# Optimization experiments

Hardware: AMD Instinct MI355X
Metric: run time of the kernel (lower is better)

Reference implementation:

```python
import jax, jax.numpy as jnp
import numpy as np

B, D, H = 256, 512, 256
K = 5
MARGIN = 1.0
TAU = 1.0
LAM_C = 0.01
LAM_E = 0.1
BETA = 0.1
LN_EPS = 1e-5


def _layernorm(x, g, b):
    mu = jnp.mean(x, axis=-1, keepdims=True)
    var = jnp.var(x, axis=-1, keepdims=True)
    return (x - mu) * jax.lax.rsqrt(var + LN_EPS) * g + b


def setup_inputs() -> dict:
    key = jax.random.key(0)
    ks = jax.random.split(key, 16)
    s = 0.02
    inp = {
        "outputs": jax.random.normal(ks[0], (B, 3, 64, 64), jnp.float32),
        "images": jax.random.normal(ks[1], (B, 3, 64, 64), jnp.float32),
        "f_orig": jax.random.normal(ks[2], (B, D), jnp.float32),
        "f_recon": jax.random.normal(ks[3], (B, D), jnp.float32),
        "cf1": jax.random.normal(ks[4], (B, 256, 8, 8), jnp.float32),
        "cf2": jax.random.normal(ks[5], (B, 512, 4, 4), jnp.float32),
        # EnergyNet encoder params
        "W1": jax.random.normal(ks[6], (D, H), jnp.float32) * s,
        "b1": jnp.zeros((H,), jnp.float32),
        "g1": jnp.ones((H,), jnp.float32),
        "be1": jnp.zeros((H,), jnp.float32),
        "W2": jax.random.normal(ks[7], (H, H), jnp.float32) * s,
        "b2": jnp.zeros((H,), jnp.float32),
        # EnergyNet interaction params
        "W3": jax.random.normal(ks[8], (3 * H, H), jnp.float32) * s,
        "b3": jnp.zeros((H,), jnp.float32),
        "g3": jnp.ones((H,), jnp.float32),
        "be3": jnp.zeros((H,), jnp.float32),
        "W4": jax.random.normal(ks[9], (H, H // 2), jnp.float32) * s,
        "b4": jnp.zeros((H // 2,), jnp.float32),
        "W5": jax.random.normal(ks[10], (H // 2, 1), jnp.float32) * s,
        "b5": jnp.zeros((1,), jnp.float32),
    }
    return inp


def _encoder(x, W1, b1, g1, be1, W2, b2):
    h = _layernorm(x @ W1 + b1, g1, be1)
    return jax.nn.relu(h) @ W2 + b2


def _energy_matrix(f1, f2, W1, b1, g1, be1, W2, b2, W3, b3, g3, be3, W4, b4, W5, b5):
    e1 = _encoder(f1, W1, b1, g1, be1, W2, b2)  # [B,H]
    e2 = _encoder(f2, W1, b1, g1, be1, W2, b2)  # [B,H]
    e1b = jnp.broadcast_to(e1[:, None, :], (B, B, H))
    e2b = jnp.broadcast_to(e2[None, :, :], (B, B, H))
    combined = jnp.concatenate([e1b, e2b, e1b * e2b], axis=-1)  # [B,B,3H]
    h = jax.nn.relu(_layernorm(combined @ W3 + b3, g3, be3))
    h = jax.nn.relu(h @ W4 + b4)
    return (h @ W5 + b5)[..., 0]  # [B,B]


def _topk_neighbors(f, k):
    fn = f / (jnp.linalg.norm(f, axis=1, keepdims=True))
    sim = fn @ fn.T
    sim = jnp.where(jnp.eye(f.shape[0], dtype=bool), -jnp.inf, sim)
    _, idx = jax.lax.top_k(sim, k)  # [B,k]
    onehot = jnp.zeros((f.shape[0], f.shape[0]), jnp.float32)
    rows = jnp.arange(f.shape[0])[:, None]
    return onehot.at[rows, idx].set(1.0)


def _entropy(x):
    xn = (x - x.min()) / (x.max() - x.min() + 1e-8)
    # torch.histc(bins=256, min=0, max=1): values at max go to last bin
    idx = jnp.clip(jnp.floor(xn.reshape(-1) * 256.0).astype(jnp.int32), 0, 255)
    hist = jnp.bincount(idx, length=256).astype(jnp.float32)
    p = hist / hist.sum()
    return -jnp.sum(p * jnp.log2(p + 1e-8))


def reference(outputs, images, f_orig, f_recon, cf1, cf2,
              W1, b1, g1, be1, W2, b2, W3, b3, g3, be3, W4, b4, W5, b5):
    # reconstruction loss
    recon = jnp.mean((outputs - images) ** 2)

    # energy margin loss
    E = _energy_matrix(f_orig, f_recon, W1, b1, g1, be1, W2, b2,
                       W3, b3, g3, be3, W4, b4, W5, b5)
    pos = jnp.diag(E)[:, None]
    losses = jax.nn.relu(MARGIN + E - pos)
    neg_mask = ~jnp.eye(B, dtype=bool)
    standard_loss = jnp.sum(losses * neg_mask) / (B * (B - 1))

    k = min(K, B - 1)
    on = _topk_neighbors(f_orig, k)
    rn = _topk_neighbors(f_recon, k)
    inter = jnp.sum(on * rn, axis=1)
    union = jnp.sum(jnp.clip(on + rn, 0.0, 1.0), axis=1)
    jaccard = inter / (union + 1e-8)
    neighbor_loss = 1.0 - jnp.mean(jaccard)
    energy_loss = standard_loss + 0.3 * neighbor_loss

    # compression loss over the dict of compressed features {cf1, cf2}
    sp = 0.5 * (jnp.mean(jnp.abs(cf1)) + jnp.mean(jnp.abs(cf2)))
    en = 0.5 * (_entropy(cf1) + _entropy(cf2))
    compress = sp + BETA * en

    total = recon + LAM_C * compress + LAM_E * energy_loss
    return (total, recon, energy_loss, compress)
```

## Files before the change

### kernel.cpp

```cpp
#include <hip/hip_runtime.h>
#include <math.h>

typedef __attribute__((ext_vector_type(8))) short short8;
typedef __attribute__((ext_vector_type(4))) float f32x4;
typedef __attribute__((ext_vector_type(4))) unsigned int u32x4;

union U8 { unsigned int u[4]; short8 s; u32x4 v; };


__device__ __forceinline__ float wave_sum(float v) {
#pragma unroll
    for (int o = 32; o > 0; o >>= 1) v += __shfl_down(v, o);
    return v;
}

__device__ __forceinline__ float block_sum256(float v, float* red) {
    v = wave_sum(v);
    int t = threadIdx.x;
    if ((t & 63) == 0) red[t >> 6] = v;
    __syncthreads();
    float r = red[0] + red[1] + red[2] + red[3];
    __syncthreads();
    return r;
}

__device__ __forceinline__ unsigned fenc(float f) {
    unsigned u = __float_as_uint(f);
    return (u & 0x80000000u) ? ~u : (u | 0x80000000u);
}
__device__ __forceinline__ float fdec(unsigned u) {
    return (u & 0x80000000u) ? __uint_as_float(u & 0x7fffffffu) : __uint_as_float(~u);
}

__device__ __forceinline__ ushort f2bf(float f) {
    unsigned u = __float_as_uint(f);
    unsigned r = (u + 0x7fffu + ((u >> 16) & 1u)) >> 16;
    return (ushort)r;
}
__device__ __forceinline__ float bflo(unsigned u) { return __uint_as_float(u << 16); }
__device__ __forceinline__ float bfhi(unsigned u) { return __uint_as_float(u & 0xffff0000u); }
__device__ __forceinline__ float bf2f(ushort u) { return __uint_as_float((unsigned)u << 16); }


__global__ void init_kernel(float* wsf, unsigned* wsu, int* wsi) {
    int t = threadIdx.x;
    if (t < 7) wsf[t] = 0.f;
    if (t == 7 || t == 9) wsu[t] = 0xFFFFFFFFu;
    if (t == 8 || t == 10) wsu[t] = 0u;
    wsi[16 + t] = 0;
    wsi[272 + t] = 0;
}

__device__ __forceinline__ void pack256(const float* __restrict__ src, ushort* __restrict__ dst, int s) {
    int lane = s & 63;
    int tt = (s >> 6) & 15;
    int kk = s >> 10;
    int qq = lane >> 4, nn = lane & 15;
    int tcol = tt * 16 + nn;
    short8 v;
#pragma unroll
    for (int jj = 0; jj < 8; ++jj) {
        int k = kk * 32 + qq * 8 + jj;
        v[jj] = (short)f2bf(src[(size_t)k * 256 + tcol]);
    }
    *(short8*)(dst + (size_t)s * 8) = v;
}

__device__ __forceinline__ void pack128(const float* __restrict__ src, ushort* __restrict__ dst, int s) {
    int lane = s & 63;
    int tt = (s >> 6) & 7;
    int kk = s >> 9;
    int qq = lane >> 4, nn = lane & 15;
    int ncol = tt * 16 + nn;
    short8 v;
#pragma unroll
    for (int jj = 0; jj < 8; ++jj) {
        int k = kk * 32 + qq * 8 + jj;
        v[jj] = (short)f2bf(src[(size_t)k * 128 + ncol]);
    }
    *(short8*)(dst + (size_t)s * 8) = v;
}

__global__ __launch_bounds__(256) void mega_kernel(
    const float4* __restrict__ o, const float4* __restrict__ im,
    const float4* __restrict__ cf1, const float4* __restrict__ cf2,
    const float* __restrict__ fo, const float* __restrict__ fr,
    const float* __restrict__ W1, const float* __restrict__ W2,
    const float* __restrict__ W3, const float* __restrict__ W4,
    float* wsf, unsigned* wsu, float* rnorm, float* fT,
    ushort* __restrict__ W3cpk, ushort* __restrict__ W4pk,
    ushort* __restrict__ W1pk, ushort* __restrict__ W2pk,
    ushort* __restrict__ W3apk, ushort* __restrict__ W3bpk) {
    __shared__ float smem[64 * 33];
    float* red = smem;
    int b = blockIdx.x, t = threadIdx.x;
    if (b < 2048) {
        if (b < 512) {
            int base = b * 1536 + t;
            float4 av[6], cv[6];
#pragma unroll
            for (int u = 0; u < 6; ++u) { av[u] = o[base + u * 256]; cv[u] = im[base + u * 256]; }
            float s0 = 0.f, s1 = 0.f;
#pragma unroll
            for (int u = 0; u < 6; ++u) {
                float dx = av[u].x - cv[u].x, dy = av[u].y - cv[u].y;
                float dz = av[u].z - cv[u].z, dw = av[u].w - cv[u].w;
                if (u & 1) s1 += dx * dx + dy * dy + dz * dz + dw * dw;
                else s0 += dx * dx + dy * dy + dz * dz + dw * dw;
            }
            float tot = block_sum256(s0 + s1, red);
            if (t == 0) atomicAdd(wsf + 0, tot);
        } else if (b < 1536) {
            int which = (b < 1024) ? 0 : 1;
            const float4* x = which ? cf2 : cf1;
            int niter = which ? 4 : 8;
            int base = which ? ((b - 1024) * 1024 + t) : ((b - 512) * 2048 + t);
            float4 v[8];
            for (int u = 0; u < niter; ++u) v[u] = x[base + u * 256];
            float s = 0.f, mn = INFINITY, mx = -INFINITY;
            for (int u = 0; u < niter; ++u) {
                float4 a = v[u];
                s += fabsf(a.x) + fabsf(a.y) + fabsf(a.z) + fabsf(a.w);
                mn = fminf(mn, fminf(fminf(a.x, a.y), fminf(a.z, a.w)));
                mx = fmaxf(mx, fmaxf(fmaxf(a.x, a.y), fmaxf(a.z, a.w)));
            }
            float tot = block_sum256(s, red);
#pragma unroll
            for (int off = 32; off > 0; off >>= 1) {
                mn = fminf(mn, __shfl_down(mn, off));
                mx = fmaxf(mx, __shfl_down(mx, off));
            }
            float* rmn = smem + 8;
            float* rmx = smem + 16;
            if ((t & 63) == 0) { rmn[t >> 6] = mn; rmx[t >> 6] = mx; }
            __syncthreads();
            if (t == 0) {
                atomicAdd(wsf + 1 + which, tot);
                float m1 = fminf(fminf(rmn[0], rmn[1]), fminf(rmn[2], rmn[3]));
                float m2 = fmaxf(fmaxf(rmx[0], rmx[1]), fmaxf(rmx[2], rmx[3]));
                atomicMin(wsu + 7 + which * 2, fenc(m1));
                atomicMax(wsu + 8 + which * 2, fenc(m2));
            }
        } else {
            int r = b - 1536;
            const float4* f = (r < 256) ? ((const float4*)fo + (size_t)r * 128)
                                        : ((const float4*)fr + (size_t)(r - 256) * 128);
            float s = 0.f;
            if (t < 128) {
                float4 a = f[t];
                s = a.x * a.x + a.y * a.y + a.z * a.z + a.w * a.w;
            }
            float tot = block_sum256(s, red);
            if (t == 0) rnorm[r] = 1.0f / sqrtf(tot);
        }
    } else if (b < 2176) {
        int bb = b - 2048;
        int pass = bb >> 6;
        int kt = (bb >> 2) & 15;
        int jt = bb & 3;
        int k0 = kt * 32, j0 = jt * 64;
        const float* f = pass ? fr : fo;
        float (*tile)[33] = (float(*)[33])smem;
        int cl = t & 31, rl = t >> 5;
#pragma unroll
        for (int r = 0; r < 8; ++r) {
            int row = j0 + rl + r * 8;
            tile[rl + r * 8][cl] = f[(size_t)row * 512 + k0 + cl];
        }
        __syncthreads();
        int jl = t & 63, kq = t >> 6;
        float* dst = fT + (size_t)pass * 131072;
#pragma unroll
        for (int c = 0; c < 8; ++c) {
            int kl = kq * 8 + c;
            dst[(size_t)(k0 + kl) * 256 + j0 + jl] = tile[jl][kl];
        }
    } else {
        int pb = b - 2176;
        if (pb < 32) pack256(W3 + 512 * 256, W3cpk, pb * 256 + t);
        else if (pb < 48) pack128(W4, W4pk, (pb - 32) * 256 + t);
        else if (pb < 112) pack256(W1, W1pk, (pb - 48) * 256 + t);
        else if (pb < 144) pack256(W2, W2pk, (pb - 112) * 256 + t);
        else if (pb < 176) pack256(W3, W3apk, (pb - 144) * 256 + t);
        else pack256(W3 + 256 * 256, W3bpk, (pb - 176) * 256 + t);
    }
}

__global__ __launch_bounds__(256) void hist_kernel(const float4* __restrict__ cf1,
                                                   const float4* __restrict__ cf2,
                                                   const unsigned* wsu, int* wsi) {
    __shared__ int hl[256];
    int b = blockIdx.x, t = threadIdx.x;
    hl[t] = 0;
    __syncthreads();
    int which = (b < 512) ? 0 : 1;
    const float4* x = which ? cf2 : cf1;
    int niter = which ? 4 : 8;
    int base = which ? ((b - 512) * 1024 + t) : (b * 2048 + t);
    int* hist = wsi + (which ? 272 : 16);
    float mn = fdec(wsu[7 + which * 2]), mx = fdec(wsu[8 + which * 2]);
    float inv = 256.f / (mx - mn + 1e-8f);
    float4 v[8];
    for (int u = 0; u < niter; ++u) v[u] = x[base + u * 256];
    for (int u = 0; u < niter; ++u) {
        float4 a = v[u];
        int b0i = min(max((int)floorf((a.x - mn) * inv), 0), 255);
        int b1i = min(max((int)floorf((a.y - mn) * inv), 0), 255);
        int b2i = min(max((int)floorf((a.z - mn) * inv), 0), 255);
        int b3i = min(max((int)floorf((a.w - mn) * inv), 0), 255);
        atomicAdd(&hl[b0i], 1);
        atomicAdd(&hl[b1i], 1);
        atomicAdd(&hl[b2i], 1);
        atomicAdd(&hl[b3i], 1);
    }
    __syncthreads();
    if (hl[t]) atomicAdd(&hist[t], hl[t]);
}

__global__ __launch_bounds__(64, 1) void encoder_mfma(
    const float* __restrict__ fo, const float* __restrict__ fr,
    const ushort* __restrict__ W1p, const ushort* __restrict__ W2p,
    const ushort* __restrict__ W3ap, const ushort* __restrict__ W3bp,
    const float* __restrict__ b1, const float* __restrict__ g1,
    const float* __restrict__ be1, const float* __restrict__ b2,
    ushort* __restrict__ ebf, ushort* __restrict__ A1bf, ushort* __restrict__ A2bf)
{
    int lane = threadIdx.x & 63;
    int q = lane >> 4, n = lane & 15;
    int r = blockIdx.x * 16 + n;
    bool isOrig = (r < 256);
    const float* f = isOrig ? (fo + (size_t)r * 512) : (fr + (size_t)(r - 256) * 512);

    f32x4 acc[16];
#pragma unroll
    for (int tt = 0; tt < 16; ++tt) acc[tt] = (f32x4){0.f, 0.f, 0.f, 0.f};
    short8 wA[16], wB[16];
    {
        const ushort* wp0 = W1p + (size_t)lane * 8;
#pragma unroll
        for (int tt = 0; tt < 16; ++tt) wA[tt] = *(const short8*)(wp0 + (size_t)tt * 512);
    }
#pragma unroll
    for (int kk = 0; kk < 16; ++kk) {
        const short8* cur = (kk & 1) ? wB : wA;
        short8* nxt = (kk & 1) ? wA : wB;
        if (kk < 15) {
            const ushort* wpn = W1p + ((size_t)((kk + 1) * 1024 + lane)) * 8;
#pragma unroll
            for (int tt = 0; tt < 16; ++tt) nxt[tt] = *(const short8*)(wpn + (size_t)tt * 512);
        }
        int kb = kk * 32 + q * 8;
        float4 fa = *(const float4*)(f + kb);
        float4 fb = *(const float4*)(f + kb + 4);
        U8 bb;
        bb.u[0] = (unsigned)f2bf(fa.x) | ((unsigned)f2bf(fa.y) << 16);
        bb.u[1] = (unsigned)f2bf(fa.z) | ((unsigned)f2bf(fa.w) << 16);
        bb.u[2] = (unsigned)f2bf(fb.x) | ((unsigned)f2bf(fb.y) << 16);
        bb.u[3] = (unsigned)f2bf(fb.z) | ((unsigned)f2bf(fb.w) << 16);
#pragma unroll
        for (int tt = 0; tt < 16; ++tt)
            acc[tt] = __builtin_amdgcn_mfma_f32_16x16x32_bf16(cur[tt], bb.s, acc[tt], 0, 0, 0);
    }
    float s1 = 0.f, s2 = 0.f;
#pragma unroll
    for (int tt = 0; tt < 16; ++tt) {
        int tb = tt * 16 + q * 4;
        float4 bv = *(const float4*)(b1 + tb);
        float v0 = acc[tt][0] + bv.x, v1 = acc[tt][1] + bv.y;
        float v2 = acc[tt][2] + bv.z, v3 = acc[tt][3] + bv.w;
        acc[tt][0] = v0; acc[tt][1] = v1; acc[tt][2] = v2; acc[tt][3] = v3;
        s1 += v0 + v1 + v2 + v3;
        s2 += v0 * v0 + v1 * v1 + v2 * v2 + v3 * v3;
    }
    s1 += __shfl_xor(s1, 16); s1 += __shfl_xor(s1, 32);
    s2 += __shfl_xor(s2, 16); s2 += __shfl_xor(s2, 32);
    float mean = s1 * (1.f / 256.f);
    float var = s2 * (1.f / 256.f) - mean * mean;
    float rstd = rsqrtf(var + 1e-5f);
    uint2 pk[16];
#pragma unroll
    for (int tt = 0; tt < 16; ++tt) {
        int tb = tt * 16 + q * 4;
        float4 gg = *(const float4*)(g1 + tb);
        float4 be = *(const float4*)(be1 + tb);
        float h0 = fmaxf((acc[tt][0] - mean) * rstd * gg.x + be.x, 0.f);
        float h1 = fmaxf((acc[tt][1] - mean) * rstd * gg.y + be.y, 0.f);
        float h2 = fmaxf((acc[tt][2] - mean) * rstd * gg.z + be.z, 0.f);
        float h3 = fmaxf((acc[tt][3] - mean) * rstd * gg.w + be.w, 0.f);
        pk[tt].x = (unsigned)f2bf(h0) | ((unsigned)f2bf(h1) << 16);
        pk[tt].y = (unsigned)f2bf(h2) | ((unsigned)f2bf(h3) << 16);
    }

    int qh = (q >> 1) & 1;
    int src0 = ((q & 1) * 2) * 16 + n;
    int src1 = src0 + 16;

    f32x4 eacc[16];
#pragma unroll
    for (int tt = 0; tt < 16; ++tt) eacc[tt] = (f32x4){0.f, 0.f, 0.f, 0.f};
    {
        const ushort* wp0 = W2p + (size_t)lane * 8;
#pragma unroll
        for (int tt = 0; tt < 16; ++tt) wA[tt] = *(const short8*)(wp0 + (size_t)tt * 512);
    }
#pragma unroll
    for (int kk = 0; kk < 8; ++kk) {
        const short8* cur = (kk & 1) ? wB : wA;
        short8* nxt = (kk & 1) ? wA : wB;
        if (kk < 7) {
            const ushort* wpn = W2p + ((size_t)((kk + 1) * 1024 + lane)) * 8;
#pragma unroll
            for (int tt = 0; tt < 16; ++tt) nxt[tt] = *(const short8*)(wpn + (size_t)tt * 512);
        }
        uint2 lo2 = pk[kk * 2], hi2 = pk[kk * 2 + 1];
        unsigned a0 = (unsigned)__shfl((int)lo2.x, src0);
        unsigned a1 = (unsigned)__shfl((int)lo2.y, src0);
        unsigned b0 = (unsigned)__shfl((int)hi2.x, src0);
        unsigned b1v = (unsigned)__shfl((int)hi2.y, src0);
        unsigned c0 = (unsigned)__shfl((int)lo2.x, src1);
        unsigned c1 = (unsigned)__shfl((int)lo2.y, src1);
        unsigned d0 = (unsigned)__shfl((int)hi2.x, src1);
        unsigned d1 = (unsigned)__shfl((int)hi2.y, src1);
        U8 hb;
        hb.u[0] = qh ? b0 : a0;
        hb.u[1] = qh ? b1v : a1;
        hb.u[2] = qh ? d0 : c0;
        hb.u[3] = qh ? d1 : c1;
#pragma unroll
        for (int tt = 0; tt < 16; ++tt)
            eacc[tt] = __builtin_amdgcn_mfma_f32_16x16x32_bf16(cur[tt], hb.s, eacc[tt], 0, 0, 0);
    }
    uint2 epk[16];
#pragma unroll
    for (int tt = 0; tt < 16; ++tt) {
        int tb = tt * 16 + q * 4;
        float4 bv = *(const float4*)(b2 + tb);
        float e0 = eacc[tt][0] + bv.x, e1 = eacc[tt][1] + bv.y;
        float e2 = eacc[tt][2] + bv.z, e3 = eacc[tt][3] + bv.w;
        epk[tt].x = (unsigned)f2bf(e0) | ((unsigned)f2bf(e1) << 16);
        epk[tt].y = (unsigned)f2bf(e2) | ((unsigned)f2bf(e3) << 16);
        *(uint2*)(ebf + (size_t)r * 256 + tb) = epk[tt];
    }

    const ushort* W3x = isOrig ? W3ap : W3bp;
    f32x4 aacc[16];
#pragma unroll
    for (int tt = 0; tt < 16; ++tt) aacc[tt] = (f32x4){0.f, 0.f, 0.f, 0.f};
    {
        const ushort* wp0 = W3x + (size_t)lane * 8;
#pragma unroll
        for (int tt = 0; tt < 16; ++tt) wA[tt] = *(const short8*)(wp0 + (size_t)tt * 512);
    }
#pragma unroll
    for (int kk = 0; kk < 8; ++kk) {
        const short8* cur = (kk & 1) ? wB : wA;
        short8* nxt = (kk & 1) ? wA : wB;
        if (kk < 7) {
            const ushort* wpn = W3x + ((size_t)((kk + 1) * 1024 + lane)) * 8;
#pragma unroll
            for (int tt = 0; tt < 16; ++tt) nxt[tt] = *(const short8*)(wpn + (size_t)tt * 512);
        }
        uint2 lo2 = epk[kk * 2], hi2 = epk[kk * 2 + 1];
        unsigned a0 = (unsigned)__shfl((int)lo2.x, src0);
        unsigned a1 = (unsigned)__shfl((int)lo2.y, src0);
        unsigned b0 = (unsigned)__shfl((int)hi2.x, src0);
        unsigned b1v = (unsigned)__shfl((int)hi2.y, src0);
        unsigned c0 = (unsigned)__shfl((int)lo2.x, src1);
        unsigned c1 = (unsigned)__shfl((int)lo2.y, src1);
        unsigned d0 = (unsigned)__shfl((int)hi2.x, src1);
        unsigned d1 = (unsigned)__shfl((int)hi2.y, src1);
        U8 hb;
        hb.u[0] = qh ? b0 : a0;
        hb.u[1] = qh ? b1v : a1;
        hb.u[2] = qh ? d0 : c0;
        hb.u[3] = qh ? d1 : c1;
#pragma unroll
        for (int tt = 0; tt < 16; ++tt)
            aacc[tt] = __builtin_amdgcn_mfma_f32_16x16x32_bf16(cur[tt], hb.s, aacc[tt], 0, 0, 0);
    }
    ushort* dst = isOrig ? (A1bf + (size_t)r * 256) : (A2bf + (size_t)(r - 256) * 256);
#pragma unroll
    for (int tt = 0; tt < 16; ++tt) {
        int tb = tt * 16 + q * 4;
        uint2 pv;
        pv.x = (unsigned)f2bf(aacc[tt][0]) | ((unsigned)f2bf(aacc[tt][1]) << 16);
        pv.y = (unsigned)f2bf(aacc[tt][2]) | ((unsigned)f2bf(aacc[tt][3]) << 16);
        *(uint2*)(dst + tb) = pv;
    }
}

__global__ __launch_bounds__(256) void simtop_kernel(const float* __restrict__ fo,
                                                     const float* __restrict__ fr,
                                                     const float* __restrict__ rnorm,
                                                     const float* __restrict__ fT,
                                                     int* __restrict__ top5) {
    int b = blockIdx.x;
    int pass = b >> 7, pair = b & 127;
    int i0 = pair * 2, i1 = i0 + 1;
    const float* f = pass ? fr : fo;
    const float* rn = rnorm + pass * 256;
    __shared__ float2 fs2[512];
    __shared__ float candV[4][2][5];
    __shared__ int candI[4][2][5];
    int t = threadIdx.x;
    const float* f0 = f + (size_t)i0 * 512;
    const float* f1 = f + (size_t)i1 * 512;
    fs2[t] = make_float2(f0[t], f1[t]);
    fs2[t + 256] = make_float2(f0[t + 256], f1[t + 256]);
    __syncthreads();
    int j = t;
    const float* col = fT + (size_t)pass * 131072 + j;
    float x0 = 0.f, x1 = 0.f, y0 = 0.f, y1 = 0.f, z0 = 0.f, z1 = 0.f, u0 = 0.f, u1 = 0.f;
#pragma unroll 8
    for (int k = 0; k < 128; ++k) {
        float v0 = col[(size_t)k * 256];
        float v1 = col[(size_t)(k + 128) * 256];
        float v2 = col[(size_t)(k + 256) * 256];
        float v3 = col[(size_t)(k + 384) * 256];
        float2 g0 = fs2[k], g1 = fs2[k + 128], g2 = fs2[k + 256], g3 = fs2[k + 384];
        x0 += g0.x * v0; x1 += g0.y * v0;
        y0 += g1.x * v1; y1 += g1.y * v1;
        z0 += g2.x * v2; z1 += g2.y * v2;
        u0 += g3.x * v3; u1 += g3.y * v3;
    }
    float a0 = ((x0 + y0) + (z0 + u0)) * rn[j];
    float a1 = ((x1 + y1) + (z1 + u1)) * rn[j];
    if (j == i0) a0 = -INFINITY;
    if (j == i1) a1 = -INFINITY;
    int w = t >> 6, lane = t & 63;
    for (int sel = 0; sel < 2; ++sel) {
        float v2 = sel ? a1 : a0;
        int idx = j;
        for (int r = 0; r < 5; ++r) {
            float m = v2;
            int mi = idx;
#pragma unroll
            for (int off = 32; off > 0; off >>= 1) {
                float om = __shfl_xor(m, off);
                int omi = __shfl_xor(mi, off);
                if (om > m || (om == m && omi < mi)) { m = om; mi = omi; }
            }
            if (lane == 0) { candV[w][sel][r] = m; candI[w][sel][r] = mi; }
            if (idx == mi) v2 = -INFINITY;
        }
    }
    __syncthreads();
    if (w < 2) {
        float v = -INFINITY;
        int ix = 0x7fffffff;
        if (lane < 20) { v = candV[lane / 5][w][lane % 5]; ix = candI[lane / 5][w][lane % 5]; }
        int iSel = w ? i1 : i0;
        for (int r = 0; r < 5; ++r) {
            float m = v;
            int mi = ix;
#pragma unroll
            for (int off = 32; off > 0; off >>= 1) {
                float om = __shfl_xor(m, off);
                int omi = __shfl_xor(mi, off);
                if (om > m || (om == m && omi < mi)) { m = om; mi = omi; }
            }
            if (lane == 0) top5[((size_t)pass * 256 + iSel) * 5 + r] = mi;
            if (ix == mi) v = -INFINITY;
        }
    }
}

__global__ __launch_bounds__(256, 2) void energy_v4(
    const ushort* __restrict__ A1bf, const ushort* __restrict__ A2bf,
    const ushort* __restrict__ ebf,
    const ushort* __restrict__ W3p, const ushort* __restrict__ W4p,
    const float* __restrict__ b3, const float* __restrict__ g3, const float* __restrict__ be3,
    const float* __restrict__ b4, const float* __restrict__ W5, const float* __restrict__ b5,
    ushort* __restrict__ E)
{
    int blk = blockIdx.x;
    int i = blk >> 1;
    int half = blk & 1;
    int t = threadIdx.x;
    int w = t >> 6, lane = t & 63, q = lane >> 4, n = lane & 15;
    int jb = half * 128 + w * 32;
    __shared__ float combS[256], g3S[256], be3S[256], b4S[128], w5S[128];
    combS[t] = bf2f(A1bf[(size_t)i * 256 + t]) + b3[t];
    g3S[t] = g3[t];
    be3S[t] = be3[t];
    if (t < 128) { b4S[t] = b4[t]; w5S[t] = W5[t]; }
    __syncthreads();

    const ushort* e1p = ebf + (size_t)i * 256;
    const ushort* e2p = ebf + 65536;

    f32x4 acc[2][16];
#pragma unroll
    for (int s = 0; s < 2; ++s)
#pragma unroll
        for (int tt = 0; tt < 16; ++tt) acc[s][tt] = (f32x4){0.f, 0.f, 0.f, 0.f};

    for (int kk = 0; kk < 8; ++kk) {
        int kbase = kk * 32 + q * 8;
        U8 e1v;
        e1v.v = *(const u32x4*)(e1p + kbase);
        float e1f[8];
#pragma unroll
        for (int x = 0; x < 4; ++x) {
            e1f[2 * x] = bflo(e1v.u[x]);
            e1f[2 * x + 1] = bfhi(e1v.u[x]);
        }
        short8 bfrag[2];
#pragma unroll
        for (int s = 0; s < 2; ++s) {
            U8 e2v;
            e2v.v = *(const u32x4*)(e2p + (size_t)(jb + s * 16 + n) * 256 + kbase);
            U8 bb;
#pragma unroll
            for (int x = 0; x < 4; ++x) {
                float p0 = bflo(e2v.u[x]) * e1f[2 * x];
                float p1 = bfhi(e2v.u[x]) * e1f[2 * x + 1];
                bb.u[x] = (unsigned)f2bf(p0) | ((unsigned)f2bf(p1) << 16);
            }
            bfrag[s] = bb.s;
        }
        const ushort* wp = W3p + ((size_t)(kk * 16) * 64 + lane) * 8;
#pragma unroll
        for (int tt = 0; tt < 16; ++tt) {
            short8 af = *(const short8*)(wp + (size_t)tt * 512);
            acc[0][tt] = __builtin_amdgcn_mfma_f32_16x16x32_bf16(af, bfrag[0], acc[0][tt], 0, 0, 0);
            acc[1][tt] = __builtin_amdgcn_mfma_f32_16x16x32_bf16(af, bfrag[1], acc[1][tt], 0, 0, 0);
        }
    }

    uint2 pk[2][16];
    float b5v = b5[0];
#pragma unroll
    for (int s = 0; s < 2; ++s) {
        int j = jb + s * 16 + n;
        float s1 = 0.f, s2 = 0.f;
#pragma unroll
        for (int tt = 0; tt < 16; ++tt) {
            int tb = tt * 16 + q * 4;
            float4 cb = *(const float4*)(combS + tb);
            uint2 a2u = *(const uint2*)(A2bf + (size_t)j * 256 + tb);
            float a0 = bflo(a2u.x), a1f = bfhi(a2u.x), a2f = bflo(a2u.y), a3f = bfhi(a2u.y);
            float v0 = acc[s][tt][0] + cb.x + a0;
            float v1 = acc[s][tt][1] + cb.y + a1f;
            float v2 = acc[s][tt][2] + cb.z + a2f;
            float v3 = acc[s][tt][3] + cb.w + a3f;
            acc[s][tt][0] = v0; acc[s][tt][1] = v1; acc[s][tt][2] = v2; acc[s][tt][3] = v3;
            s1 += v0 + v1 + v2 + v3;
            s2 += v0 * v0 + v1 * v1 + v2 * v2 + v3 * v3;
        }
        s1 += __shfl_xor(s1, 16); s1 += __shfl_xor(s1, 32);
        s2 += __shfl_xor(s2, 16); s2 += __shfl_xor(s2, 32);
        float mean = s1 * (1.f / 256.f);
        float var = s2 * (1.f / 256.f) - mean * mean;
        float rstd = rsqrtf(var + 1e-5f);
#pragma unroll
        for (int tt = 0; tt < 16; ++tt) {
            int tb = tt * 16 + q * 4;
            float4 gg = *(const float4*)(g3S + tb);
            float4 be = *(const float4*)(be3S + tb);
            float h0 = fmaxf((acc[s][tt][0] - mean) * rstd * gg.x + be.x, 0.f);
            float h1 = fmaxf((acc[s][tt][1] - mean) * rstd * gg.y + be.y, 0.f);
            float h2 = fmaxf((acc[s][tt][2] - mean) * rstd * gg.z + be.z, 0.f);
            float h3 = fmaxf((acc[s][tt][3] - mean) * rstd * gg.w + be.w, 0.f);
            pk[s][tt].x = (unsigned)f2bf(h0) | ((unsigned)f2bf(h1) << 16);
            pk[s][tt].y = (unsigned)f2bf(h2) | ((unsigned)f2bf(h3) << 16);
        }
    }

    f32x4 gacc[2][8];
#pragma unroll
    for (int s = 0; s < 2; ++s)
#pragma unroll
        for (int nt = 0; nt < 8; ++nt) gacc[s][nt] = (f32x4){0.f, 0.f, 0.f, 0.f};

    int qh = (q >> 1) & 1;
    int src0 = ((q & 1) * 2) * 16 + n;
    int src1 = src0 + 16;
#pragma unroll
    for (int kk = 0; kk < 8; ++kk) {
        const ushort* wp = W4p + ((size_t)(kk * 8) * 64 + lane) * 8;
#pragma unroll
        for (int s = 0; s < 2; ++s) {
            uint2 lo2 = pk[s][kk * 2], hi2 = pk[s][kk * 2 + 1];
            unsigned a0 = (unsigned)__shfl((int)lo2.x, src0);
            unsigned a1 = (unsigned)__shfl((int)lo2.y, src0);
            unsigned b0 = (unsigned)__shfl((int)hi2.x, src0);
            unsigned b1 = (unsigned)__shfl((int)hi2.y, src0);
            unsigned c0 = (unsigned)__shfl((int)lo2.x, src1);
            unsigned c1 = (unsigned)__shfl((int)lo2.y, src1);
            unsigned d0 = (unsigned)__shfl((int)hi2.x, src1);
            unsigned d1 = (unsigned)__shfl((int)hi2.y, src1);
            U8 hb;
            hb.u[0] = qh ? b0 : a0;
            hb.u[1] = qh ? b1 : a1;
            hb.u[2] = qh ? d0 : c0;
            hb.u[3] = qh ? d1 : c1;
#pragma unroll
            for (int nt = 0; nt < 8; ++nt) {
                short8 wa = *(const short8*)(wp + (size_t)nt * 512);
                gacc[s][nt] = __builtin_amdgcn_mfma_f32_16x16x32_bf16(wa, hb.s, gacc[s][nt], 0, 0, 0);
            }
        }
    }

#pragma unroll
    for (int s = 0; s < 2; ++s) {
        float ep = 0.f;
#pragma unroll
        for (int nt = 0; nt < 8; ++nt) {
            int nb = nt * 16 + q * 4;
            float4 b4v = *(const float4*)(b4S + nb);
            float4 w5v = *(const float4*)(w5S + nb);
            ep += fmaxf(gacc[s][nt][0] + b4v.x, 0.f) * w5v.x;
            ep += fmaxf(gacc[s][nt][1] + b4v.y, 0.f) * w5v.y;
            ep += fmaxf(gacc[s][nt][2] + b4v.z, 0.f) * w5v.z;
            ep += fmaxf(gacc[s][nt][3] + b4v.w, 0.f) * w5v.w;
        }
        ep += __shfl_xor(ep, 16);
        ep += __shfl_xor(ep, 32);
        if (q == 0) E[(size_t)i * 256 + jb + s * 16 + n] = f2bf(ep + b5v);
    }
}

__global__ void margin_jac_kernel(const ushort* __restrict__ E, const int* __restrict__ top5,
                                  float* slAcc, float* jacOut) {
    __shared__ float red[4];
    int b = blockIdx.x, t = threadIdx.x;
    if (b < 256) {
        float diag = bf2f(E[(size_t)b * 256 + b]);
        float l = (t == b) ? 0.f : fmaxf(1.f + bf2f(E[(size_t)b * 256 + t]) - diag, 0.f);
        float tot = block_sum256(l, red);
        if (t == 0) atomicAdd(slAcc, tot);
    } else {
        int O[5], R[5];
#pragma unroll
        for (int r = 0; r < 5; ++r) {
            O[r] = top5[t * 5 + r];
            R[r] = top5[(256 + t) * 5 + r];
        }
        int inter = 0;
#pragma unroll
        for (int a = 0; a < 5; ++a)
#pragma unroll
            for (int bq = 0; bq < 5; ++bq) inter += (O[a] == R[bq]);
        float fi2 = (float)inter;
        float jac = fi2 / (10.f - fi2 + 1e-8f);
        float s = block_sum256(jac, red);
        if (t == 0) jacOut[0] = s;
    }
}

__global__ void finalize_kernel(const float* wsf, const int* h1, const int* h2, float* out) {
    __shared__ float red[4];
    int t = threadIdx.x;
    float p1 = (float)h1[t] / 4194304.f;
    float p2 = (float)h2[t] / 2097152.f;
    float s1 = block_sum256(-p1 * log2f(p1 + 1e-8f), red);
    float s2 = block_sum256(-p2 * log2f(p2 + 1e-8f), red);
    if (t == 0) {
        float recon = wsf[0] / 3145728.f;
        float sp = 0.5f * (wsf[1] / 4194304.f + wsf[2] / 2097152.f);
        float en = 0.5f * (s1 + s2);
        float compress = sp + 0.1f * en;
        float sl = wsf[5] / (256.f * 255.f);
        float nl = 1.f - wsf[6] / 256.f;
        float energy = sl + 0.3f * nl;
        float total = recon + 0.01f * compress + 0.1f * energy;
        out[0] = total;
        out[1] = recon;
        out[2] = energy;
        out[3] = compress;
    }
}

extern "C" void kernel_launch(void* const* d_in, const int* in_sizes, int n_in,
                              void* d_out, int out_size, void* d_ws, size_t ws_size,
                              hipStream_t stream) {
    const float* outputs = (const float*)d_in[0];
    const float* images  = (const float*)d_in[1];
    const float* f_orig  = (const float*)d_in[2];
    const float* f_recon = (const float*)d_in[3];
    const float* cf1 = (const float*)d_in[4];
    const float* cf2 = (const float*)d_in[5];
    const float* W1 = (const float*)d_in[6];
    const float* b1 = (const float*)d_in[7];
    const float* g1 = (const float*)d_in[8];
    const float* be1 = (const float*)d_in[9];
    const float* W2 = (const float*)d_in[10];
    const float* b2 = (const float*)d_in[11];
    const float* W3 = (const float*)d_in[12];
    const float* b3 = (const float*)d_in[13];
    const float* g3 = (const float*)d_in[14];
    const float* be3 = (const float*)d_in[15];
    const float* W4 = (const float*)d_in[16];
    const float* b4 = (const float*)d_in[17];
    const float* W5 = (const float*)d_in[18];
    const float* b5 = (const float*)d_in[19];

    float* wsf = (float*)d_ws;
    unsigned* wsu = (unsigned*)d_ws;
    int* wsi = (int*)d_ws;
    float* out = (float*)d_out;

    float* rnorm = wsf + 528;
    ushort* A1bf = (ushort*)(wsf + 1040);
    ushort* A2bf = (ushort*)(wsf + 33808);
    ushort* ebf  = (ushort*)(wsf + 66576);
    ushort* Ebf  = (ushort*)(wsf + 132112);
    ushort* W3cpk = (ushort*)(wsf + 164880);
    ushort* W4pk  = (ushort*)(wsf + 197648);
    ushort* W1pk  = (ushort*)(wsf + 214032);
    ushort* W2pk  = (ushort*)(wsf + 279568);
    ushort* W3apk = (ushort*)(wsf + 312336);
    ushort* W3bpk = (ushort*)(wsf + 345104);
    float* fT = wsf + 377872;
    int* top5 = wsi + 640016;

    hipLaunchKernelGGL(init_kernel, dim3(1), dim3(256), 0, stream, wsf, wsu, wsi);
    hipLaunchKernelGGL(mega_kernel, dim3(2384), dim3(256), 0, stream,
                       (const float4*)outputs, (const float4*)images,
                       (const float4*)cf1, (const float4*)cf2,
                       f_orig, f_recon, W1, W2, W3, W4,
                       wsf, wsu, rnorm, fT, W3cpk, W4pk, W1pk, W2pk, W3apk, W3bpk);
    hipLaunchKernelGGL(hist_kernel, dim3(1024), dim3(256), 0, stream,
                       (const float4*)cf1, (const float4*)cf2, wsu, wsi);
    hipLaunchKernelGGL(encoder_mfma, dim3(32), dim3(64), 0, stream,
                       f_orig, f_recon, W1pk, W2pk, W3apk, W3bpk,
                       b1, g1, be1, b2, ebf, A1bf, A2bf);
    hipLaunchKernelGGL(simtop_kernel, dim3(256), dim3(256), 0, stream,
                       f_orig, f_recon, rnorm, fT, top5);
    hipLaunchKernelGGL(energy_v4, dim3(512), dim3(256), 0, stream,
                       A1bf, A2bf, ebf, W3cpk, W4pk, b3, g3, be3, b4, W5, b5, Ebf);
    hipLaunchKernelGGL(margin_jac_kernel, dim3(257), dim3(256), 0, stream,
                       Ebf, top5, wsf + 5, wsf + 6);
    hipLaunchKernelGGL(finalize_kernel, dim3(1), dim3(256), 0, stream,
                       wsf, wsi + 16, wsi + 272, out);
}
```

Before: 277.8 us.

## Stage W3c in LDS and process both column halves per energy block

The energy kernel now stages the packed 256x256 bf16 W3c slice (128 KB) into shared memory once per block. Each block then handles a full row i by looping over both column halves, halving the grid to 256 blocks and reading the MFMA A-operand from LDS instead of global/L2. W4 fragments are hoisted into registers per k-step. The mega kernel is reordered so the weight-packing and transpose blocks come first. The cost is one block per CU because of the large LDS footprint, lower occupancy, and a 128 KB preload per block.

Measured after the change: 330.2 us. 18.9% more time.

```diff
diff --git a/kernel.cpp b/kernel.cpp
--- a/kernel.cpp
+++ b/kernel.cpp
@@ -94,9 +94,40 @@
     __shared__ float smem[64 * 33];
     float* red = smem;
     int b = blockIdx.x, t = threadIdx.x;
-    if (b < 2048) {
-        if (b < 512) {
-            int base = b * 1536 + t;
+    if (b < 208) {
+        int pb = b;
+        if (pb < 32) pack256(W3 + 512 * 256, W3cpk, pb * 256 + t);
+        else if (pb < 48) pack128(W4, W4pk, (pb - 32) * 256 + t);
+        else if (pb < 112) pack256(W1, W1pk, (pb - 48) * 256 + t);
+        else if (pb < 144) pack256(W2, W2pk, (pb - 112) * 256 + t);
+        else if (pb < 176) pack256(W3, W3apk, (pb - 144) * 256 + t);
+        else pack256(W3 + 256 * 256, W3bpk, (pb - 176) * 256 + t);
+    } else if (b < 336) {
+        int bb = b - 208;
+        int pass = bb >> 6;
+        int kt = (bb >> 2) & 15;
+        int jt = bb & 3;
+        int k0 = kt * 32, j0 = jt * 64;
+        const float* f = pass ? fr : fo;
+        float (*tile)[33] = (float(*)[33])smem;
+        int cl = t & 31, rl = t >> 5;
+#pragma unroll
+        for (int r = 0; r < 8; ++r) {
+            int row = j0 + rl + r * 8;
+            tile[rl + r * 8][cl] = f[(size_t)row * 512 + k0 + cl];
+        }
+        __syncthreads();
+        int jl = t & 63, kq = t >> 6;
+        float* dst = fT + (size_t)pass * 131072;
+#pragma unroll
+        for (int c = 0; c < 8; ++c) {
+            int kl = kq * 8 + c;
+            dst[(size_t)(k0 + kl) * 256 + j0 + jl] = tile[jl][kl];
+        }
+    } else {
+        int bs = b - 336;
+        if (bs < 512) {
+            int base = bs * 1536 + t;
             float4 av[6], cv[6];
 #pragma unroll
             for (int u = 0; u < 6; ++u) { av[u] = o[base + u * 256]; cv[u] = im[base + u * 256]; }
@@ -110,11 +141,11 @@
             }
             float tot = block_sum256(s0 + s1, red);
             if (t == 0) atomicAdd(wsf + 0, tot);
-        } else if (b < 1536) {
-            int which = (b < 1024) ? 0 : 1;
+        } else if (bs < 1536) {
+            int which = (bs < 1024) ? 0 : 1;
             const float4* x = which ? cf2 : cf1;
             int niter = which ? 4 : 8;
-            int base = which ? ((b - 1024) * 1024 + t) : ((b - 512) * 2048 + t);
+            int base = which ? ((bs - 1024) * 1024 + t) : ((bs - 512) * 2048 + t);
             float4 v[8];
             for (int u = 0; u < niter; ++u) v[u] = x[base + u * 256];
             float s = 0.f, mn = INFINITY, mx = -INFINITY;
@@ -142,7 +173,7 @@
                 atomicMax(wsu + 8 + which * 2, fenc(m2));
             }
         } else {
-            int r = b - 1536;
+            int r = bs - 1536;
             const float4* f = (r < 256) ? ((const float4*)fo + (size_t)r * 128)
                                         : ((const float4*)fr + (size_t)(r - 256) * 128);
             float s = 0.f;
@@ -153,36 +184,6 @@
             float tot = block_sum256(s, red);
             if (t == 0) rnorm[r] = 1.0f / sqrtf(tot);
         }
-    } else if (b < 2176) {
-        int bb = b - 2048;
-        int pass = bb >> 6;
-        int kt = (bb >> 2) & 15;
-        int jt = bb & 3;
-        int k0 = kt * 32, j0 = jt * 64;
-        const float* f = pass ? fr : fo;
-        float (*tile)[33] = (float(*)[33])smem;
-        int cl = t & 31, rl = t >> 5;
-#pragma unroll
-        for (int r = 0; r < 8; ++r) {
-            int row = j0 + rl + r * 8;
-            tile[rl + r * 8][cl] = f[(size_t)row * 512 + k0 + cl];
-        }
-        __syncthreads();
-        int jl = t & 63, kq = t >> 6;
-        float* dst = fT + (size_t)pass * 131072;
-#pragma unroll
-        for (int c = 0; c < 8; ++c) {
-            int kl = kq * 8 + c;
-            dst[(size_t)(k0 + kl) * 256 + j0 + jl] = tile[jl][kl];
-        }
-    } else {
-        int pb = b - 2176;
-        if (pb < 32) pack256(W3 + 512 * 256, W3cpk, pb * 256 + t);
-        else if (pb < 48) pack128(W4, W4pk, (pb - 32) * 256 + t);
-        else if (pb < 112) pack256(W1, W1pk, (pb - 48) * 256 + t);
-        else if (pb < 144) pack256(W2, W2pk, (pb - 112) * 256 + t);
-        else if (pb < 176) pack256(W3, W3apk, (pb - 144) * 256 + t);
-        else pack256(W3 + 256 * 256, W3bpk, (pb - 176) * 256 + t);
     }
 }
 
@@ -465,7 +466,7 @@
     }
 }
 
-__global__ __launch_bounds__(256, 2) void energy_v4(
+__global__ __launch_bounds__(256, 1) void energy_v5(
     const ushort* __restrict__ A1bf, const ushort* __restrict__ A2bf,
     const ushort* __restrict__ ebf,
     const ushort* __restrict__ W3p, const ushort* __restrict__ W4p,
@@ -473,13 +474,18 @@
     const float* __restrict__ b4, const float* __restrict__ W5, const float* __restrict__ b5,
     ushort* __restrict__ E)
 {
-    int blk = blockIdx.x;
-    int i = blk >> 1;
-    int half = blk & 1;
+    int i = blockIdx.x;
     int t = threadIdx.x;
     int w = t >> 6, lane = t & 63, q = lane >> 4, n = lane & 15;
-    int jb = half * 128 + w * 32;
+    __shared__ __align__(16) ushort W3s[65536];
     __shared__ float combS[256], g3S[256], be3S[256], b4S[128], w5S[128];
+
+    {
+        const uint4* src = (const uint4*)W3p;
+        uint4* dstl = (uint4*)W3s;
+#pragma unroll
+        for (int x = 0; x < 32; ++x) dstl[x * 256 + t] = src[x * 256 + t];
+    }
     combS[t] = bf2f(A1bf[(size_t)i * 256 + t]) + b3[t];
     g3S[t] = g3[t];
     be3S[t] = be3[t];
@@ -488,137 +494,142 @@
 
     const ushort* e1p = ebf + (size_t)i * 256;
     const ushort* e2p = ebf + 65536;
-
-    f32x4 acc[2][16];
-#pragma unroll
-    for (int s = 0; s < 2; ++s)
-#pragma unroll
-        for (int tt = 0; tt < 16; ++tt) acc[s][tt] = (f32x4){0.f, 0.f, 0.f, 0.f};
-
-    for (int kk = 0; kk < 8; ++kk) {
-        int kbase = kk * 32 + q * 8;
-        U8 e1v;
-        e1v.v = *(const u32x4*)(e1p + kbase);
-        float e1f[8];
-#pragma unroll
-        for (int x = 0; x < 4; ++x) {
-            e1f[2 * x] = bflo(e1v.u[x]);
-            e1f[2 * x + 1] = bfhi(e1v.u[x]);
-        }
-        short8 bfrag[2];
-#pragma unroll
-        for (int s = 0; s < 2; ++s) {
-            U8 e2v;
-            e2v.v = *(const u32x4*)(e2p + (size_t)(jb + s * 16 + n) * 256 + kbase);
-            U8 bb;
-#pragma unroll
-            for (int x = 0; x < 4; ++x) {
-                float p0 = bflo(e2v.u[x]) * e1f[2 * x];
-                float p1 = bfhi(e2v.u[x]) * e1f[2 * x + 1];
-                bb.u[x] = (unsigned)f2bf(p0) | ((unsigned)f2bf(p1) << 16);
-            }
-            bfrag[s] = bb.s;
-        }
-        const ushort* wp = W3p + ((size_t)(kk * 16) * 64 + lane) * 8;
-#pragma unroll
-        for (int tt = 0; tt < 16; ++tt) {
-            short8 af = *(const short8*)(wp + (size_t)tt * 512);
-            acc[0][tt] = __builtin_amdgcn_mfma_f32_16x16x32_bf16(af, bfrag[0], acc[0][tt], 0, 0, 0);
-            acc[1][tt] = __builtin_amdgcn_mfma_f32_16x16x32_bf16(af, bfrag[1], acc[1][tt], 0, 0, 0);
-        }
-    }
-
-    uint2 pk[2][16];
     float b5v = b5[0];
-#pragma unroll
-    for (int s = 0; s < 2; ++s) {
-        int j = jb + s * 16 + n;
-        float s1 = 0.f, s2 = 0.f;
-#pragma unroll
-        for (int tt = 0; tt < 16; ++tt) {
-            int tb = tt * 16 + q * 4;
-            float4 cb = *(const float4*)(combS + tb);
-            uint2 a2u = *(const uint2*)(A2bf + (size_t)j * 256 + tb);
-            float a0 = bflo(a2u.x), a1f = bfhi(a2u.x), a2f = bflo(a2u.y), a3f = bfhi(a2u.y);
-            float v0 = acc[s][tt][0] + cb.x + a0;
-            float v1 = acc[s][tt][1] + cb.y + a1f;
-            float v2 = acc[s][tt][2] + cb.z + a2f;
-            float v3 = acc[s][tt][3] + cb.w + a3f;
-            acc[s][tt][0] = v0; acc[s][tt][1] = v1; acc[s][tt][2] = v2; acc[s][tt][3] = v3;
-            s1 += v0 + v1 + v2 + v3;
-            s2 += v0 * v0 + v1 * v1 + v2 * v2 + v3 * v3;
-        }
-        s1 += __shfl_xor(s1, 16); s1 += __shfl_xor(s1, 32);
-        s2 += __shfl_xor(s2, 16); s2 += __shfl_xor(s2, 32);
-        float mean = s1 * (1.f / 256.f);
-        float var = s2 * (1.f / 256.f) - mean * mean;
-        float rstd = rsqrtf(var + 1e-5f);
-#pragma unroll
-        for (int tt = 0; tt < 16; ++tt) {
-            int tb = tt * 16 + q * 4;
-            float4 gg = *(const float4*)(g3S + tb);
-            float4 be = *(const float4*)(be3S + tb);
-            float h0 = fmaxf((acc[s][tt][0] - mean) * rstd * gg.x + be.x, 0.f);
-            float h1 = fmaxf((acc[s][tt][1] - mean) * rstd * gg.y + be.y, 0.f);
-            float h2 = fmaxf((acc[s][tt][2] - mean) * rstd * gg.z + be.z, 0.f);
-            float h3 = fmaxf((acc[s][tt][3] - mean) * rstd * gg.w + be.w, 0.f);
-            pk[s][tt].x = (unsigned)f2bf(h0) | ((unsigned)f2bf(h1) << 16);
-            pk[s][tt].y = (unsigned)f2bf(h2) | ((unsigned)f2bf(h3) << 16);
-        }
-    }
-
-    f32x4 gacc[2][8];
-#pragma unroll
-    for (int s = 0; s < 2; ++s)
-#pragma unroll
-        for (int nt = 0; nt < 8; ++nt) gacc[s][nt] = (f32x4){0.f, 0.f, 0.f, 0.f};
-
     int qh = (q >> 1) & 1;
     int src0 = ((q & 1) * 2) * 16 + n;
     int src1 = src0 + 16;
-#pragma unroll
-    for (int kk = 0; kk < 8; ++kk) {
-        const ushort* wp = W4p + ((size_t)(kk * 8) * 64 + lane) * 8;
+
+    for (int half = 0; half < 2; ++half) {
+        int jb = half * 128 + w * 32;
+
+        f32x4 acc[2][16];
+#pragma unroll
+        for (int s = 0; s < 2; ++s)
+#pragma unroll
+            for (int tt = 0; tt < 16; ++tt) acc[s][tt] = (f32x4){0.f, 0.f, 0.f, 0.f};
+
+        for (int kk = 0; kk < 8; ++kk) {
+            int kbase = kk * 32 + q * 8;
+            U8 e1v;
+            e1v.v = *(const u32x4*)(e1p + kbase);
+            float e1f[8];
+#pragma unroll
+            for (int x = 0; x < 4; ++x) {
+                e1f[2 * x] = bflo(e1v.u[x]);
+                e1f[2 * x + 1] = bfhi(e1v.u[x]);
+            }
+            short8 bfrag[2];
+#pragma unroll
+            for (int s = 0; s < 2; ++s) {
+                U8 e2v;
+                e2v.v = *(const u32x4*)(e2p + (size_t)(jb + s * 16 + n) * 256 + kbase);
+                U8 bb;
+#pragma unroll
+                for (int x = 0; x < 4; ++x) {
+                    float p0 = bflo(e2v.u[x]) * e1f[2 * x];
+                    float p1 = bfhi(e2v.u[x]) * e1f[2 * x + 1];
+                    bb.u[x] = (unsigned)f2bf(p0) | ((unsigned)f2bf(p1) << 16);
+                }
+                bfrag[s] = bb.s;
+            }
+            const ushort* wp = W3s + ((size_t)(kk * 16) * 64 + lane) * 8;
+#pragma unroll
+            for (int tt = 0; tt < 16; ++tt) {
+                short8 af = *(const short8*)(wp + (size_t)tt * 512);
+                acc[0][tt] = __builtin_amdgcn_mfma_f32_16x16x32_bf16(af, bfrag[0], acc[0][tt], 0, 0, 0);
+                acc[1][tt] = __builtin_amdgcn_mfma_f32_16x16x32_bf16(af, bfrag[1], acc[1][tt], 0, 0, 0);
+            }
+        }
+
+        uint2 pk[2][16];
 #pragma unroll
         for (int s = 0; s < 2; ++s) {
-            uint2 lo2 = pk[s][kk * 2], hi2 = pk[s][kk * 2 + 1];
-            unsigned a0 = (unsigned)__shfl((int)lo2.x, src0);
-            unsigned a1 = (unsigned)__shfl((int)lo2.y, src0);
-            unsigned b0 = (unsigned)__shfl((int)hi2.x, src0);
-            unsigned b1 = (unsigned)__shfl((int)hi2.y, src0);
-            unsigned c0 = (unsigned)__shfl((int)lo2.x, src1);
-            unsigned c1 = (unsigned)__shfl((int)lo2.y, src1);
-            unsigned d0 = (unsigned)__shfl((int)hi2.x, src1);
-            unsigned d1 = (unsigned)__shfl((int)hi2.y, src1);
-            U8 hb;
-            hb.u[0] = qh ? b0 : a0;
-            hb.u[1] = qh ? b1 : a1;
-            hb.u[2] = qh ? d0 : c0;
-            hb.u[3] = qh ? d1 : c1;
+            int j = jb + s * 16 + n;
+            float s1 = 0.f, s2 = 0.f;
+#pragma unroll
+            for (int tt = 0; tt < 16; ++tt) {
+                int tb = tt * 16 + q * 4;
+                float4 cb = *(const float4*)(combS + tb);
+                uint2 a2u = *(const uint2*)(A2bf + (size_t)j * 256 + tb);
+                float a0 = bflo(a2u.x), a1f = bfhi(a2u.x), a2f = bflo(a2u.y), a3f = bfhi(a2u.y);
+                float v0 = acc[s][tt][0] + cb.x + a0;
+                float v1 = acc[s][tt][1] + cb.y + a1f;
+                float v2 = acc[s][tt][2] + cb.z + a2f;
+                float v3 = acc[s][tt][3] + cb.w + a3f;
+                acc[s][tt][0] = v0; acc[s][tt][1] = v1; acc[s][tt][2] = v2; acc[s][tt][3] = v3;
+                s1 += v0 + v1 + v2 + v3;
+                s2 += v0 * v0 + v1 * v1 + v2 * v2 + v3 * v3;
+            }
+            s1 += __shfl_xor(s1, 16); s1 += __shfl_xor(s1, 32);
+            s2 += __shfl_xor(s2, 16); s2 += __shfl_xor(s2, 32);
+            float mean = s1 * (1.f / 256.f);
+            float var = s2 * (1.f / 256.f) - mean * mean;
+            float rstd = rsqrtf(var + 1e-5f);
+#pragma unroll
+            for (int tt = 0; tt < 16; ++tt) {
+                int tb = tt * 16 + q * 4;
+                float4 gg = *(const float4*)(g3S + tb);
+                float4 be = *(const float4*)(be3S + tb);
+                float h0 = fmaxf((acc[s][tt][0] - mean) * rstd * gg.x + be.x, 0.f);
+                float h1 = fmaxf((acc[s][tt][1] - mean) * rstd * gg.y + be.y, 0.f);
+                float h2 = fmaxf((acc[s][tt][2] - mean) * rstd * gg.z + be.z, 0.f);
+                float h3 = fmaxf((acc[s][tt][3] - mean) * rstd * gg.w + be.w, 0.f);
+                pk[s][tt].x = (unsigned)f2bf(h0) | ((unsigned)f2bf(h1) << 16);
+                pk[s][tt].y = (unsigned)f2bf(h2) | ((unsigned)f2bf(h3) << 16);
+            }
+        }
+
+        f32x4 gacc[2][8];
+#pragma unroll
+        for (int s = 0; s < 2; ++s)
+#pragma unroll
+            for (int nt = 0; nt < 8; ++nt) gacc[s][nt] = (f32x4){0.f, 0.f, 0.f, 0.f};
+
+#pragma unroll
+        for (int kk = 0; kk < 8; ++kk) {
+            short8 wa[8];
+            const ushort* wp = W4p + ((size_t)(kk * 8) * 64 + lane) * 8;
+#pragma unroll
+            for (int nt = 0; nt < 8; ++nt) wa[nt] = *(const short8*)(wp + (size_t)nt * 512);
+#pragma unroll
+            for (int s = 0; s < 2; ++s) {
+                uint2 lo2 = pk[s][kk * 2], hi2 = pk[s][kk * 2 + 1];
+                unsigned a0 = (unsigned)__shfl((int)lo2.x, src0);
+                unsigned a1 = (unsigned)__shfl((int)lo2.y, src0);
+                unsigned b0 = (unsigned)__shfl((int)hi2.x, src0);
+                unsigned b1 = (unsigned)__shfl((int)hi2.y, src0);
+                unsigned c0 = (unsigned)__shfl((int)lo2.x, src1);
+                unsigned c1 = (unsigned)__shfl((int)lo2.y, src1);
+                unsigned d0 = (unsigned)__shfl((int)hi2.x, src1);
+                unsigned d1 = (unsigned)__shfl((int)hi2.y, src1);
+                U8 hb;
+                hb.u[0] = qh ? b0 : a0;
+                hb.u[1] = qh ? b1 : a1;
+                hb.u[2] = qh ? d0 : c0;
+                hb.u[3] = qh ? d1 : c1;
+#pragma unroll
+                for (int nt = 0; nt < 8; ++nt)
+                    gacc[s][nt] = __builtin_amdgcn_mfma_f32_16x16x32_bf16(wa[nt], hb.s, gacc[s][nt], 0, 0, 0);
+            }
+        }
+
+#pragma unroll
+        for (int s = 0; s < 2; ++s) {
+            float ep = 0.f;
 #pragma unroll
             for (int nt = 0; nt < 8; ++nt) {
-                short8 wa = *(const short8*)(wp + (size_t)nt * 512);
-                gacc[s][nt] = __builtin_amdgcn_mfma_f32_16x16x32_bf16(wa, hb.s, gacc[s][nt], 0, 0, 0);
-            }
-        }
-    }
-
-#pragma unroll
-    for (int s = 0; s < 2; ++s) {
-        float ep = 0.f;
-#pragma unroll
-        for (int nt = 0; nt < 8; ++nt) {
-            int nb = nt * 16 + q * 4;
-            float4 b4v = *(const float4*)(b4S + nb);
-            float4 w5v = *(const float4*)(w5S + nb);
-            ep += fmaxf(gacc[s][nt][0] + b4v.x, 0.f) * w5v.x;
-            ep += fmaxf(gacc[s][nt][1] + b4v.y, 0.f) * w5v.y;
-            ep += fmaxf(gacc[s][nt][2] + b4v.z, 0.f) * w5v.z;
-            ep += fmaxf(gacc[s][nt][3] + b4v.w, 0.f) * w5v.w;
-        }
-        ep += __shfl_xor(ep, 16);
-        ep += __shfl_xor(ep, 32);
-        if (q == 0) E[(size_t)i * 256 + jb + s * 16 + n] = f2bf(ep + b5v);
+                int nb = nt * 16 + q * 4;
+                float4 b4v = *(const float4*)(b4S + nb);
+                float4 w5v = *(const float4*)(w5S + nb);
+                ep += fmaxf(gacc[s][nt][0] + b4v.x, 0.f) * w5v.x;
+                ep += fmaxf(gacc[s][nt][1] + b4v.y, 0.f) * w5v.y;
+                ep += fmaxf(gacc[s][nt][2] + b4v.z, 0.f) * w5v.z;
+                ep += fmaxf(gacc[s][nt][3] + b4v.w, 0.f) * w5v.w;
+            }
+            ep += __shfl_xor(ep, 16);
+            ep += __shfl_xor(ep, 32);
+            if (q == 0) E[(size_t)i * 256 + jb + s * 16 + n] = f2bf(ep + b5v);
+        }
     }
 }
 
@@ -729,7 +740,7 @@
                        b1, g1, be1, b2, ebf, A1bf, A2bf);
     hipLaunchKernelGGL(simtop_kernel, dim3(256), dim3(256), 0, stream,
                        f_orig, f_recon, rnorm, fT, top5);
-    hipLaunchKernelGGL(energy_v4, dim3(512), dim3(256), 0, stream,
+    hipLaunchKernelGGL(energy_v5, dim3(256), dim3(256), 0, stream,
                        A1bf, A2bf, ebf, W3cpk, W4pk, b3, g3, be3, b4, W5, b5, Ebf);
     hipLaunchKernelGGL(margin_jac_kernel, dim3(257), dim3(256), 0, stream,
                        Ebf, top5, wsf + 5, wsf + 6);
```
